# Kernel optimization log

Hardware: AMD Instinct MI355X
Metric: run time of the kernel (lower is better)

The kernel has to match this reference:

```python
import jax, jax.numpy as jnp
import numpy as np

INV_SQRT_4PI = 0.28209479177387814  # 1/sqrt(4*pi)

def sh_l(r, l):
    """Real spherical harmonics of unit vectors r [..., 3], e3nn order,
    'integral' normalization (e3nn o3.spherical_harmonics default)."""
    x, y, z = r[..., 0], r[..., 1], r[..., 2]
    if l == 0:
        return jnp.full(r.shape[:-1] + (1,), INV_SQRT_4PI, r.dtype)
    if l == 1:
        return 0.4886025119029199 * r  # sqrt(3/(4pi)) * (x, y, z)
    s15 = 3.872983346207417 * INV_SQRT_4PI   # sqrt(15)/sqrt(4pi)
    s5 = 2.23606797749979 * INV_SQRT_4PI     # sqrt(5)/sqrt(4pi)
    return jnp.stack([
        s15 * x * z,
        s15 * x * y,
        s5 * (y * y - 0.5 * (x * x + z * z)),
        s15 * y * z,
        0.5 * s15 * (z * z - x * x),
    ], axis=-1)

def layer_norm(x, g, b, eps=1e-5):
    mu = jnp.mean(x, axis=-1, keepdims=True)
    var = jnp.mean((x - mu) ** 2, axis=-1, keepdims=True)
    return (x - mu) * jax.lax.rsqrt(var + eps) * g + b

def setup_inputs() -> dict:
    key = jax.random.key(0)
    N, C, L = 1024, 128, 3  # nodes, sphere_channels, lmax+1
    ks = jax.random.split(key, 12)
    s = 0.02
    return {
        "x_emb": jax.random.normal(ks[0], (N, 9, C), jnp.float32),
        "pos": jax.random.normal(ks[1], (N, 3), jnp.float32) * 3.0,
        "q_w": jax.random.normal(ks[2], (C, C), jnp.float32) * s,
        "q_b": jnp.zeros((C,), jnp.float32),
        "k_w": jax.random.normal(ks[3], (C, C), jnp.float32) * s,
        "k_b": jnp.zeros((C,), jnp.float32),
        "v_w": jax.random.normal(ks[4], (L, C, C), jnp.float32) * s,
        "v_b0": jnp.zeros((C,), jnp.float32),
        "out_w": jax.random.normal(ks[5], (L, C, C), jnp.float32) * s,
        "ln_g": jnp.ones((L, C), jnp.float32),
        "ln_b": jnp.zeros((L, C), jnp.float32),
        "batch": jnp.sort(jax.random.randint(ks[6], (N,), 0, 16)).astype(jnp.int64),
    }

def reference(x_emb, pos, q_w, q_b, k_w, k_b, v_w, v_b0, out_w, ln_g, ln_b, batch):
    N, _, C = x_emb.shape
    H = 8
    D = C // H
    degs = (1, 3, 5)  # 2l+1 for l = 0, 1, 2

    # pairwise unit displacements  [N, N, 3]
    diff = pos[:, None, :] - pos[None, :, :]
    dist = jnp.maximum(jnp.linalg.norm(diff, axis=-1, keepdims=True), 1e-8)
    r_hat = diff / dist

    same = batch[:, None] == batch[None, :]           # [N, N]
    valid = same & ~jnp.eye(N, dtype=bool)

    # per-degree features: split x_emb[:, 9, C] into [1, 3, 5]
    feats = [x_emb[:, 0:1], x_emb[:, 1:4], x_emb[:, 4:9]]

    # HTR invariant pairwise score  [N, N, C]
    score = jnp.zeros((N, N, C), x_emb.dtype)
    for l, f in enumerate(feats):
        sh = sh_l(r_hat, l)                           # [N, N, 2l+1]
        score = score + jnp.einsum('imc,ijm->ijc', f, sh) / degs[l]
    score = score * valid[..., None].astype(score.dtype)

    q = (score.mean(axis=1) @ q_w.T + q_b).reshape(N, H, D)
    k = (score.mean(axis=0) @ k_w.T + k_b).reshape(N, H, D)

    attn = jnp.einsum('ihd,jhd->hij', q, k) * (D ** -0.5)
    attn = jnp.where(same[None], attn, -jnp.inf)
    attn = jnp.nan_to_num(jax.nn.softmax(attn, axis=-1))

    outs = []
    for l, f in enumerate(feats):
        m = degs[l]
        v = f @ v_w[l].T
        if l == 0:
            v = v + v_b0
        v = v.reshape(N, m, H, D)
        o = jnp.einsum('hij,jmhd->imhd', attn, v).reshape(N, m, C)
        o = o @ out_w[l].T
        outs.append(layer_norm(f + o, ln_g[l], ln_b[l]))
    return jnp.concatenate(outs, axis=1)
```

## Files before the change

kernel.cpp:

```cpp
#include <hip/hip_runtime.h>
#include <hip/hip_bf16.h>
#include <math.h>

#define NN 1024

typedef __attribute__((ext_vector_type(8))) short bf16x8;
typedef __attribute__((ext_vector_type(4))) float f32x4;

__device__ __forceinline__ float wave_sum(float v) {
#pragma unroll
  for (int off = 32; off > 0; off >>= 1) v += __shfl_down(v, off);
  return v;
}
__device__ __forceinline__ float wave_max(float v) {
#pragma unroll
  for (int off = 32; off > 0; off >>= 1) v = fmaxf(v, __shfl_down(v, off));
  return v;
}
__device__ __forceinline__ short f2bf(float x) {
  __hip_bfloat16 b = __float2bfloat16(x);
  return *(short*)&b;
}

#define SH_C0 0.28209479177387814f
#define SH_C1 0.4886025119029199f
#define SH_S15 1.0925484305920792f
#define SH_S5 0.6307831305050401f

__global__ __launch_bounds__(256) void htr_geom(
    const float* __restrict__ qw, const float* __restrict__ kw,
    const float* __restrict__ vw, const float* __restrict__ ow,
    const float* __restrict__ x_emb, const float* __restrict__ pos,
    const int* __restrict__ batch, short* __restrict__ wbf,
    short* __restrict__ x_bf, short* __restrict__ fT,
    short* __restrict__ Wsh, short* __restrict__ rowm_bf) {
  const int b = blockIdx.x;
  const int tid = threadIdx.x;
  __shared__ short tile[128][34];
  __shared__ float red[4][9];
  __shared__ float sm[9];

  if (b < 8) {
    const float* src;
    if (b == 0) src = qw;
    else if (b == 1) src = kw;
    else if (b < 5) src = vw + (b - 2) * 16384;
    else src = ow + (b - 5) * 16384;
    short* dst = wbf + b * 16384;
    for (int idx = tid; idx < 16384; idx += 256) dst[idx] = f2bf(src[idx]);
  } else if (b < 1160) {
    int base = (b - 8) * 1024 + tid * 4;
    float4 v = *(const float4*)(x_emb + base);
    *(short4*)(x_bf + base) = make_short4(f2bf(v.x), f2bf(v.y), f2bf(v.z), f2bf(v.w));
  } else if (b < 1448) {
    const int sub = b - 1160;
    const int i0 = (sub & 31) * 32;
    const int m = sub >> 5;
#pragma unroll
    for (int it = 0; it < 16; ++it) {
      int e = tid + it * 256;
      int r = e >> 7, c = e & 127;
      tile[c][r] = f2bf(x_emb[((i0 + r) * 9 + m) * 128 + c]);
    }
    __syncthreads();
#pragma unroll
    for (int it = 0; it < 8; ++it) {
      int idx = tid + it * 256;
      int c = idx >> 4, ii2 = idx & 15;
      *(short2*)(fT + c * 9216 + m * 1024 + i0 + ii2 * 2) =
          make_short2(tile[c][ii2 * 2], tile[c][ii2 * 2 + 1]);
    }
  } else if (b < 2472) {
    const int j = b - 1448;
    const float pjx = pos[j * 3 + 0], pjy = pos[j * 3 + 1], pjz = pos[j * 3 + 2];
    const int bj = batch[j];
    short* wrow = Wsh + j * 9216;
    for (int i = tid; i < 1024; i += 256) {
      float dx = pos[i * 3 + 0] - pjx;
      float dy = pos[i * 3 + 1] - pjy;
      float dz = pos[i * 3 + 2] - pjz;
      bool ok = (i != j) && (batch[i] == bj);
      float okf = ok ? 1.f : 0.f;
      float d2 = dx * dx + dy * dy + dz * dz;
      float inv = okf / fmaxf(sqrtf(d2), 1e-8f);
      float x = dx * inv, y = dy * inv, z = dz * inv;
      wrow[0 * 1024 + i] = f2bf(SH_C0 * okf);
      wrow[1 * 1024 + i] = f2bf((SH_C1 * (1.f / 3.f)) * x);
      wrow[2 * 1024 + i] = f2bf((SH_C1 * (1.f / 3.f)) * y);
      wrow[3 * 1024 + i] = f2bf((SH_C1 * (1.f / 3.f)) * z);
      wrow[4 * 1024 + i] = f2bf((SH_S15 * 0.2f) * x * z);
      wrow[5 * 1024 + i] = f2bf((SH_S15 * 0.2f) * x * y);
      wrow[6 * 1024 + i] = f2bf((SH_S5 * 0.2f) * (y * y - 0.5f * (x * x + z * z)));
      wrow[7 * 1024 + i] = f2bf((SH_S15 * 0.2f) * y * z);
      wrow[8 * 1024 + i] = f2bf((0.5f * SH_S15 * 0.2f) * (z * z - x * x));
    }
  } else {
    const int i = b - 2472;
    const float px = pos[i * 3 + 0], py = pos[i * 3 + 1], pz = pos[i * 3 + 2];
    const int bi = batch[i];
    float s[9];
#pragma unroll
    for (int m = 0; m < 9; ++m) s[m] = 0.f;
    for (int j = tid; j < NN; j += 256) {
      if (j == i) continue;
      if (batch[j] != bi) continue;
      float dx = px - pos[j * 3 + 0];
      float dy = py - pos[j * 3 + 1];
      float dz = pz - pos[j * 3 + 2];
      float d2 = dx * dx + dy * dy + dz * dz;
      float inv = 1.0f / fmaxf(sqrtf(d2), 1e-8f);
      float x = dx * inv, y = dy * inv, z = dz * inv;
      s[0] += 1.0f;
      s[1] += x; s[2] += y; s[3] += z;
      s[4] += x * z; s[5] += x * y;
      s[6] += y * y - 0.5f * (x * x + z * z);
      s[7] += y * z;
      s[8] += z * z - x * x;
    }
    const int wave = tid >> 6, lane = tid & 63;
#pragma unroll
    for (int m = 0; m < 9; ++m) {
      float v = wave_sum(s[m]);
      if (lane == 0) red[wave][m] = v;
    }
    __syncthreads();
    if (tid < 9) {
      float v = red[0][tid] + red[1][tid] + red[2][tid] + red[3][tid];
      float scl = SH_S15 * 0.2f;
      if (tid == 0) scl = SH_C0;
      else if (tid < 4) scl = SH_C1 * (1.f / 3.f);
      else if (tid == 6) scl = SH_S5 * 0.2f;
      else if (tid == 8) scl = 0.5f * SH_S15 * 0.2f;
      sm[tid] = v * scl * (1.0f / 1024.0f);
    }
    __syncthreads();
    if (tid < 128) {
      float acc = 0.f;
#pragma unroll
      for (int m = 0; m < 9; ++m)
        acc = fmaf(sm[m], x_emb[(i * 9 + m) * 128 + tid], acc);
      rowm_bf[i * 128 + tid] = f2bf(acc);
    }
  }
}

#define CMS 16
__global__ __launch_bounds__(64) void htr_colmean_mfma(
    const short* __restrict__ Wsh, const short* __restrict__ fT,
    float* __restrict__ part) {
  const int jbase = blockIdx.x * 16;
  const int ks = blockIdx.y;
  const int lane = threadIdx.x;
  const int q = lane >> 4, l15 = lane & 15;
  const short* ap = Wsh + (jbase + l15) * 9216 + ks * 576 + q * 8;
  const short* bp = fT + l15 * 9216 + ks * 576 + q * 8;
  f32x4 acc[8];
#pragma unroll
  for (int t = 0; t < 8; ++t) acc[t] = (f32x4){0.f, 0.f, 0.f, 0.f};
  bf16x8 a = *(const bf16x8*)ap;
  bf16x8 b[8];
#pragma unroll
  for (int t = 0; t < 8; ++t) b[t] = *(const bf16x8*)(bp + t * 147456);
  for (int s = 1; s < 18; ++s) {
    const int off = s * 32;
    bf16x8 an = *(const bf16x8*)(ap + off);
    bf16x8 bn[8];
#pragma unroll
    for (int t = 0; t < 8; ++t) bn[t] = *(const bf16x8*)(bp + t * 147456 + off);
#pragma unroll
    for (int t = 0; t < 8; ++t)
      acc[t] = __builtin_amdgcn_mfma_f32_16x16x32_bf16(a, b[t], acc[t], 0, 0, 0);
    a = an;
#pragma unroll
    for (int t = 0; t < 8; ++t) b[t] = bn[t];
  }
#pragma unroll
  for (int t = 0; t < 8; ++t)
    acc[t] = __builtin_amdgcn_mfma_f32_16x16x32_bf16(a, b[t], acc[t], 0, 0, 0);
#pragma unroll
  for (int t = 0; t < 8; ++t)
#pragma unroll
    for (int r = 0; r < 4; ++r)
      part[(ks * 1024 + jbase + q * 4 + r) * 128 + t * 16 + l15] = acc[t][r];
}

__global__ __launch_bounds__(64) void htr_proj(
    const short* __restrict__ rowm_bf, const float* __restrict__ part,
    const short* __restrict__ x_bf, const short* __restrict__ wbf,
    const float* __restrict__ q_b, const float* __restrict__ k_b,
    const float* __restrict__ v_b0, float* __restrict__ qbuf,
    float* __restrict__ khbuf, short* __restrict__ vbT) {
  const int ibase = blockIdx.x * 16;
  const int y = blockIdx.y;
  const int lane = threadIdx.x;
  const int q = lane >> 4, l15 = lane & 15;

  bf16x8 a[4];
  const short* bp;
  if (y == 0) {
    const short* ap = rowm_bf + (ibase + l15) * 128 + q * 8;
#pragma unroll
    for (int ks = 0; ks < 4; ++ks) a[ks] = *(const bf16x8*)(ap + ks * 32);
    bp = wbf + l15 * 128 + q * 8;
  } else if (y == 1) {
    const float* pp = part + (size_t)(ibase + l15) * 128;
#pragma unroll
    for (int ks = 0; ks < 4; ++ks) {
      float s0 = 0.f, s1 = 0.f, s2 = 0.f, s3 = 0.f;
      float s4 = 0.f, s5 = 0.f, s6 = 0.f, s7 = 0.f;
#pragma unroll
      for (int s = 0; s < CMS; ++s) {
        const float* ps = pp + s * 131072 + ks * 32 + q * 8;
        float4 u0 = *(const float4*)(ps);
        float4 u1 = *(const float4*)(ps + 4);
        s0 += u0.x; s1 += u0.y; s2 += u0.z; s3 += u0.w;
        s4 += u1.x; s5 += u1.y; s6 += u1.z; s7 += u1.w;
      }
      const float sc = 1.0f / 1024.0f;
      bf16x8 av;
      av[0] = f2bf(s0 * sc); av[1] = f2bf(s1 * sc);
      av[2] = f2bf(s2 * sc); av[3] = f2bf(s3 * sc);
      av[4] = f2bf(s4 * sc); av[5] = f2bf(s5 * sc);
      av[6] = f2bf(s6 * sc); av[7] = f2bf(s7 * sc);
      a[ks] = av;
    }
    bp = wbf + 16384 + l15 * 128 + q * 8;
  } else {
    const int m = y - 2;
    const int l = (m == 0) ? 0 : ((m < 4) ? 1 : 2);
    const short* ap = x_bf + ((ibase + l15) * 9 + m) * 128 + q * 8;
#pragma unroll
    for (int ks = 0; ks < 4; ++ks) a[ks] = *(const bf16x8*)(ap + ks * 32);
    bp = wbf + (2 + l) * 16384 + l15 * 128 + q * 8;
  }

  f32x4 acc[8];
#pragma unroll
  for (int t = 0; t < 8; ++t) {
    acc[t] = (f32x4){0.f, 0.f, 0.f, 0.f};
    const short* bt = bp + t * 2048;
#pragma unroll
    for (int ks = 0; ks < 4; ++ks) {
      bf16x8 b = *(const bf16x8*)(bt + ks * 32);
      acc[t] = __builtin_amdgcn_mfma_f32_16x16x32_bf16(a[ks], b, acc[t], 0, 0, 0);
    }
  }

  if (y == 0) {
#pragma unroll
    for (int t = 0; t < 8; ++t) {
      float bo = q_b[t * 16 + l15];
#pragma unroll
      for (int r = 0; r < 4; ++r)
        qbuf[(ibase + q * 4 + r) * 128 + t * 16 + l15] = acc[t][r] + bo;
    }
  } else if (y == 1) {
#pragma unroll
    for (int t = 0; t < 8; ++t) {
      float bo = k_b[t * 16 + l15];
#pragma unroll
      for (int r = 0; r < 4; ++r)
        khbuf[(t * 1024 + ibase + q * 4 + r) * 16 + l15] = acc[t][r] + bo;
    }
  } else {
    const int m = y - 2;
#pragma unroll
    for (int t = 0; t < 8; ++t) {
      float bias = (m == 0) ? v_b0[t * 16 + l15] : 0.f;
#pragma unroll
      for (int r = 0; r < 4; ++r)
        vbT[(t * 144 + m * 16 + l15) * 1024 + ibase + q * 4 + r] =
            f2bf(acc[t][r] + bias);
    }
  }
}

template <int NT0, int NT>
__device__ __forceinline__ void apply_phase(
    const short* P, const short* __restrict__ vbT,
    short* __restrict__ obuf_bf, int ibase, int h, int lane) {
  const int q = lane >> 4, l15 = lane & 15;
  const int xs = (l15 & 7) << 3;
  const short* pr = P + l15 * 1024;
  const short* bp = vbT + (h * 144 + l15) * 1024 + q * 8;
  f32x4 acc[NT];
#pragma unroll
  for (int t = 0; t < NT; ++t) acc[t] = (f32x4){0.f, 0.f, 0.f, 0.f};
  bf16x8 a = *(const bf16x8*)(pr + ((q * 8) ^ xs));
  bf16x8 b[NT];
#pragma unroll
  for (int t = 0; t < NT; ++t) b[t] = *(const bf16x8*)(bp + (NT0 + t) * 16384);
  for (int ks = 1; ks < 32; ++ks) {
    const int off = ks * 32;
    bf16x8 an = *(const bf16x8*)(pr + ((off + q * 8) ^ xs));
    bf16x8 bn[NT];
#pragma unroll
    for (int t = 0; t < NT; ++t)
      bn[t] = *(const bf16x8*)(bp + (NT0 + t) * 16384 + off);
#pragma unroll
    for (int t = 0; t < NT; ++t)
      acc[t] = __builtin_amdgcn_mfma_f32_16x16x32_bf16(a, b[t], acc[t], 0, 0, 0);
    a = an;
#pragma unroll
    for (int t = 0; t < NT; ++t) b[t] = bn[t];
  }
#pragma unroll
  for (int t = 0; t < NT; ++t)
    acc[t] = __builtin_amdgcn_mfma_f32_16x16x32_bf16(a, b[t], acc[t], 0, 0, 0);
#pragma unroll
  for (int t = 0; t < NT; ++t)
#pragma unroll
    for (int r = 0; r < 4; ++r)
      obuf_bf[((ibase + q * 4 + r) * 9 + NT0 + t) * 128 + h * 16 + l15] =
          f2bf(acc[t][r]);
}

__global__ __launch_bounds__(256) void htr_attn_apply(
    const float* __restrict__ qbuf, const float* __restrict__ khbuf,
    const int* __restrict__ batch, const short* __restrict__ vbT,
    short* __restrict__ obuf_bf) {
  const int ibase = blockIdx.x * 16;
  const int h = blockIdx.y;
  const int tid = threadIdx.x;
  const int w = tid >> 6;
  const int lane = tid & 63;
  __shared__ short P[16 * 1024];

  const int r0 = ibase + w * 4;
  float qr[4][16];
  int bi[4];
#pragma unroll
  for (int r = 0; r < 4; ++r) {
    bi[r] = batch[r0 + r];
    const float* qp = qbuf + (r0 + r) * 128 + h * 16;
#pragma unroll
    for (int d = 0; d < 16; ++d) qr[r][d] = qp[d] * 0.25f;
  }
  float s[4][16];
#pragma unroll
  for (int jt = 0; jt < 16; ++jt) {
    const int j = jt * 64 + lane;
    const int bj = batch[j];
    const float4* kp = (const float4*)(khbuf + (h * 1024 + j) * 16);
    float4 k0 = kp[0], k1 = kp[1], k2 = kp[2], k3 = kp[3];
#pragma unroll
    for (int r = 0; r < 4; ++r) {
      float d = 0.f;
      d = fmaf(qr[r][0], k0.x, d);  d = fmaf(qr[r][1], k0.y, d);
      d = fmaf(qr[r][2], k0.z, d);  d = fmaf(qr[r][3], k0.w, d);
      d = fmaf(qr[r][4], k1.x, d);  d = fmaf(qr[r][5], k1.y, d);
      d = fmaf(qr[r][6], k1.z, d);  d = fmaf(qr[r][7], k1.w, d);
      d = fmaf(qr[r][8], k2.x, d);  d = fmaf(qr[r][9], k2.y, d);
      d = fmaf(qr[r][10], k2.z, d); d = fmaf(qr[r][11], k2.w, d);
      d = fmaf(qr[r][12], k3.x, d); d = fmaf(qr[r][13], k3.y, d);
      d = fmaf(qr[r][14], k3.z, d); d = fmaf(qr[r][15], k3.w, d);
      s[r][jt] = (bj == bi[r]) ? d : -INFINITY;
    }
  }
#pragma unroll
  for (int r = 0; r < 4; ++r) {
    float mx = s[r][0];
#pragma unroll
    for (int jt = 1; jt < 16; ++jt) mx = fmaxf(mx, s[r][jt]);
    mx = wave_max(mx);
    mx = __shfl(mx, 0);
    float t = 0.f;
#pragma unroll
    for (int jt = 0; jt < 16; ++jt) {
      s[r][jt] = expf(s[r][jt] - mx);
      t += s[r][jt];
    }
    t = wave_sum(t);
    t = __shfl(t, 0);
    const float inv = 1.0f / t;
    const int row = w * 4 + r;
    const int xs = (row & 7) << 3;
    short* pw = P + row * 1024;
#pragma unroll
    for (int jt = 0; jt < 16; ++jt) {
      const int j = jt * 64 + lane;
      pw[j ^ xs] = f2bf(s[r][jt] * inv);
    }
  }
  __syncthreads();

  if (w == 0)      apply_phase<0, 3>(P, vbT, obuf_bf, ibase, h, lane);
  else if (w == 1) apply_phase<3, 2>(P, vbT, obuf_bf, ibase, h, lane);
  else if (w == 2) apply_phase<5, 2>(P, vbT, obuf_bf, ibase, h, lane);
  else             apply_phase<7, 2>(P, vbT, obuf_bf, ibase, h, lane);
}

__global__ __launch_bounds__(64) void htr_outln_mfma(
    const short* __restrict__ obuf_bf, const float* __restrict__ x_emb,
    const short* __restrict__ wbf, const float* __restrict__ ln_g,
    const float* __restrict__ ln_b, float* __restrict__ out) {
  const int ibase = blockIdx.x * 16;
  const int m = blockIdx.y;
  const int l = (m == 0) ? 0 : ((m < 4) ? 1 : 2);
  const int lane = threadIdx.x;
  const int q = lane >> 4, l15 = lane & 15;
  const short* ap = obuf_bf + ((ibase + l15) * 9 + m) * 128 + q * 8;
  const short* bp = wbf + (5 + l) * 16384 + l15 * 128 + q * 8;
  bf16x8 a[4];
#pragma unroll
  for (int ks = 0; ks < 4; ++ks) a[ks] = *(const bf16x8*)(ap + ks * 32);
  f32x4 acc[8];
#pragma unroll
  for (int t = 0; t < 8; ++t) {
    acc[t] = (f32x4){0.f, 0.f, 0.f, 0.f};
    const short* bt = bp + t * 2048;
#pragma unroll
    for (int ks = 0; ks < 4; ++ks) {
      bf16x8 b = *(const bf16x8*)(bt + ks * 32);
      acc[t] = __builtin_amdgcn_mfma_f32_16x16x32_bf16(a[ks], b, acc[t], 0, 0, 0);
    }
  }
  float g[8], bb[8];
#pragma unroll
  for (int t = 0; t < 8; ++t) {
    g[t] = ln_g[l * 128 + t * 16 + l15];
    bb[t] = ln_b[l * 128 + t * 16 + l15];
  }
#pragma unroll
  for (int r = 0; r < 4; ++r) {
    const int i = ibase + q * 4 + r;
    const float* xr = x_emb + (i * 9 + m) * 128;
    float v[8];
    float sv = 0.f, sq = 0.f;
#pragma unroll
    for (int t = 0; t < 8; ++t) {
      v[t] = acc[t][r] + xr[t * 16 + l15];
      sv += v[t];
      sq += v[t] * v[t];
    }
#pragma unroll
    for (int off = 1; off < 16; off <<= 1) {
      sv += __shfl_xor(sv, off);
      sq += __shfl_xor(sq, off);
    }
    float mu = sv * (1.f / 128.f);
    float var = sq * (1.f / 128.f) - mu * mu;
    float rs = rsqrtf(var + 1e-5f);
    float* orow = out + (i * 9 + m) * 128;
#pragma unroll
    for (int t = 0; t < 8; ++t)
      orow[t * 16 + l15] = (v[t] - mu) * rs * g[t] + bb[t];
  }
}

extern "C" void kernel_launch(void* const* d_in, const int* in_sizes, int n_in,
                              void* d_out, int out_size, void* d_ws, size_t ws_size,
                              hipStream_t stream) {
  (void)in_sizes; (void)n_in; (void)out_size; (void)ws_size;
  const float* x_emb = (const float*)d_in[0];
  const float* pos   = (const float*)d_in[1];
  const float* q_w   = (const float*)d_in[2];
  const float* q_b   = (const float*)d_in[3];
  const float* k_w   = (const float*)d_in[4];
  const float* k_b   = (const float*)d_in[5];
  const float* v_w   = (const float*)d_in[6];
  const float* v_b0  = (const float*)d_in[7];
  const float* out_w = (const float*)d_in[8];
  const float* ln_g  = (const float*)d_in[9];
  const float* ln_b  = (const float*)d_in[10];
  const int*   batch = (const int*)d_in[11];
  float* out = (float*)d_out;

  float* ws = (float*)d_ws;
  short* rowm_bf = (short*)(ws + 0);
  float* qbuf    = ws + 65536;
  float* khbuf   = ws + 196608;
  short* wbf     = (short*)(ws + 327680);
  short* x_bf    = (short*)(ws + 393216);
  short* vbT     = (short*)(ws + 983040);
  short* obuf_bf = (short*)(ws + 1572864);
  float* part    = ws + 2162688;
  short* Wsh     = (short*)(ws + 6356992);
  short* fT      = (short*)(ws + 11075584);

  htr_geom<<<3496, 256, 0, stream>>>(q_w, k_w, v_w, out_w, x_emb, pos, batch,
                                     wbf, x_bf, fT, Wsh, rowm_bf);
  htr_colmean_mfma<<<dim3(64, CMS), 64, 0, stream>>>(Wsh, fT, part);
  htr_proj<<<dim3(64, 11), 64, 0, stream>>>(rowm_bf, part, x_bf, wbf, q_b, k_b,
                                            v_b0, qbuf, khbuf, vbT);
  htr_attn_apply<<<dim3(64, 8), 256, 0, stream>>>(qbuf, khbuf, batch, vbT,
                                                  obuf_bf);
  htr_outln_mfma<<<dim3(64, 9), 64, 0, stream>>>(obuf_bf, x_emb, wbf, ln_g,
                                                 ln_b, out);
}
```

Before: 157.7 us.

## Compute spherical-harmonic weights on the fly inside column-mean MFMA kernel

Measured after the change: 192.2 us. 21.8% more time.

```diff
diff --git a/kernel.cpp b/kernel.cpp
--- a/kernel.cpp
+++ b/kernel.cpp
@@ -33,7 +33,7 @@
     const float* __restrict__ x_emb, const float* __restrict__ pos,
     const int* __restrict__ batch, short* __restrict__ wbf,
     short* __restrict__ x_bf, short* __restrict__ fT,
-    short* __restrict__ Wsh, short* __restrict__ rowm_bf) {
+    short* __restrict__ rowm_bf) {
   const int b = blockIdx.x;
   const int tid = threadIdx.x;
   __shared__ short tile[128][34];
@@ -70,32 +70,8 @@
       *(short2*)(fT + c * 9216 + m * 1024 + i0 + ii2 * 2) =
           make_short2(tile[c][ii2 * 2], tile[c][ii2 * 2 + 1]);
     }
-  } else if (b < 2472) {
-    const int j = b - 1448;
-    const float pjx = pos[j * 3 + 0], pjy = pos[j * 3 + 1], pjz = pos[j * 3 + 2];
-    const int bj = batch[j];
-    short* wrow = Wsh + j * 9216;
-    for (int i = tid; i < 1024; i += 256) {
-      float dx = pos[i * 3 + 0] - pjx;
-      float dy = pos[i * 3 + 1] - pjy;
-      float dz = pos[i * 3 + 2] - pjz;
-      bool ok = (i != j) && (batch[i] == bj);
-      float okf = ok ? 1.f : 0.f;
-      float d2 = dx * dx + dy * dy + dz * dz;
-      float inv = okf / fmaxf(sqrtf(d2), 1e-8f);
-      float x = dx * inv, y = dy * inv, z = dz * inv;
-      wrow[0 * 1024 + i] = f2bf(SH_C0 * okf);
-      wrow[1 * 1024 + i] = f2bf((SH_C1 * (1.f / 3.f)) * x);
-      wrow[2 * 1024 + i] = f2bf((SH_C1 * (1.f / 3.f)) * y);
-      wrow[3 * 1024 + i] = f2bf((SH_C1 * (1.f / 3.f)) * z);
-      wrow[4 * 1024 + i] = f2bf((SH_S15 * 0.2f) * x * z);
-      wrow[5 * 1024 + i] = f2bf((SH_S15 * 0.2f) * x * y);
-      wrow[6 * 1024 + i] = f2bf((SH_S5 * 0.2f) * (y * y - 0.5f * (x * x + z * z)));
-      wrow[7 * 1024 + i] = f2bf((SH_S15 * 0.2f) * y * z);
-      wrow[8 * 1024 + i] = f2bf((0.5f * SH_S15 * 0.2f) * (z * z - x * x));
-    }
   } else {
-    const int i = b - 2472;
+    const int i = b - 1448;
     const float px = pos[i * 3 + 0], py = pos[i * 3 + 1], pz = pos[i * 3 + 2];
     const int bi = batch[i];
     float s[9];
@@ -146,37 +122,86 @@
 
 #define CMS 16
 __global__ __launch_bounds__(64) void htr_colmean_mfma(
-    const short* __restrict__ Wsh, const short* __restrict__ fT,
-    float* __restrict__ part) {
+    const float* __restrict__ pos, const int* __restrict__ batch,
+    const short* __restrict__ fT, float* __restrict__ part) {
   const int jbase = blockIdx.x * 16;
   const int ks = blockIdx.y;
   const int lane = threadIdx.x;
   const int q = lane >> 4, l15 = lane & 15;
-  const short* ap = Wsh + (jbase + l15) * 9216 + ks * 576 + q * 8;
+  __shared__ float4 pb[1024];
+  for (int i = lane; i < 1024; i += 64)
+    pb[i] = make_float4(pos[i * 3 + 0], pos[i * 3 + 1], pos[i * 3 + 2],
+                        __int_as_float(batch[i]));
+  __syncthreads();
+
+  const int j = jbase + l15;
+  const float4 pj = pb[j];
+  const int bj = __float_as_int(pj.w);
   const short* bp = fT + l15 * 9216 + ks * 576 + q * 8;
+
   f32x4 acc[8];
 #pragma unroll
   for (int t = 0; t < 8; ++t) acc[t] = (f32x4){0.f, 0.f, 0.f, 0.f};
-  bf16x8 a = *(const bf16x8*)ap;
   bf16x8 b[8];
 #pragma unroll
   for (int t = 0; t < 8; ++t) b[t] = *(const bf16x8*)(bp + t * 147456);
-  for (int s = 1; s < 18; ++s) {
-    const int off = s * 32;
-    bf16x8 an = *(const bf16x8*)(ap + off);
+
+  for (int s = 0; s < 18; ++s) {
     bf16x8 bn[8];
-#pragma unroll
-    for (int t = 0; t < 8; ++t) bn[t] = *(const bf16x8*)(bp + t * 147456 + off);
+    if (s < 17) {
+      const int off = (s + 1) * 32;
+#pragma unroll
+      for (int t = 0; t < 8; ++t) bn[t] = *(const bf16x8*)(bp + t * 147456 + off);
+    }
+    const int k0 = ks * 576 + s * 32;
+    const int m = k0 >> 10;
+    const int ib = (k0 & 1023) + q * 8;
+    bf16x8 av;
+    if (m == 0) {
+#pragma unroll
+      for (int t = 0; t < 8; ++t) {
+        const int e = (t + q) & 7;
+        const int i = ib + e;
+        const float4 pi = pb[i];
+        const bool ok = (i != j) && (__float_as_int(pi.w) == bj);
+        av[e] = f2bf(SH_C0 * (ok ? 1.f : 0.f));
+      }
+    } else {
+#pragma unroll
+      for (int t = 0; t < 8; ++t) {
+        const int e = (t + q) & 7;
+        const int i = ib + e;
+        const float4 pi = pb[i];
+        const bool ok = (i != j) && (__float_as_int(pi.w) == bj);
+        const float okf = ok ? 1.f : 0.f;
+        const float dx = pi.x - pj.x;
+        const float dy = pi.y - pj.y;
+        const float dz = pi.z - pj.z;
+        const float d2 = dx * dx + dy * dy + dz * dz;
+        const float inv = okf / fmaxf(sqrtf(d2), 1e-8f);
+        const float x = dx * inv, y = dy * inv, z = dz * inv;
+        float v;
+        switch (m) {
+          case 1: v = (SH_C1 * (1.f / 3.f)) * x; break;
+          case 2: v = (SH_C1 * (1.f / 3.f)) * y; break;
+          case 3: v = (SH_C1 * (1.f / 3.f)) * z; break;
+          case 4: v = (SH_S15 * 0.2f) * x * z; break;
+          case 5: v = (SH_S15 * 0.2f) * x * y; break;
+          case 6: v = (SH_S5 * 0.2f) * (y * y - 0.5f * (x * x + z * z)); break;
+          case 7: v = (SH_S15 * 0.2f) * y * z; break;
+          default: v = (0.5f * SH_S15 * 0.2f) * (z * z - x * x); break;
+        }
+        av[e] = f2bf(v);
+      }
+    }
 #pragma unroll
     for (int t = 0; t < 8; ++t)
-      acc[t] = __builtin_amdgcn_mfma_f32_16x16x32_bf16(a, b[t], acc[t], 0, 0, 0);
-    a = an;
-#pragma unroll
-    for (int t = 0; t < 8; ++t) b[t] = bn[t];
-  }
-#pragma unroll
-  for (int t = 0; t < 8; ++t)
-    acc[t] = __builtin_amdgcn_mfma_f32_16x16x32_bf16(a, b[t], acc[t], 0, 0, 0);
+      acc[t] = __builtin_amdgcn_mfma_f32_16x16x32_bf16(av, b[t], acc[t], 0, 0, 0);
+    if (s < 17) {
+#pragma unroll
+      for (int t = 0; t < 8; ++t) b[t] = bn[t];
+    }
+  }
 #pragma unroll
   for (int t = 0; t < 8; ++t)
 #pragma unroll
@@ -475,12 +500,11 @@
   short* vbT     = (short*)(ws + 983040);
   short* obuf_bf = (short*)(ws + 1572864);
   float* part    = ws + 2162688;
-  short* Wsh     = (short*)(ws + 6356992);
   short* fT      = (short*)(ws + 11075584);
 
-  htr_geom<<<3496, 256, 0, stream>>>(q_w, k_w, v_w, out_w, x_emb, pos, batch,
-                                     wbf, x_bf, fT, Wsh, rowm_bf);
-  htr_colmean_mfma<<<dim3(64, CMS), 64, 0, stream>>>(Wsh, fT, part);
+  htr_geom<<<2472, 256, 0, stream>>>(q_w, k_w, v_w, out_w, x_emb, pos, batch,
+                                     wbf, x_bf, fT, rowm_bf);
+  htr_colmean_mfma<<<dim3(64, CMS), 64, 0, stream>>>(pos, batch, fT, part);
   htr_proj<<<dim3(64, 11), 64, 0, stream>>>(rowm_bf, part, x_bf, wbf, q_b, k_b,
                                             v_b0, qbuf, khbuf, vbT);
   htr_attn_apply<<<dim3(64, 8), 256, 0, stream>>>(qbuf, khbuf, batch, vbT,
```

## Stage shared B tile in LDS across four waves in colmean MFMA kernel

Applied to the files above, without the earlier changes.

After: 152.7 us. 3.2% less time.

```diff
diff --git a/kernel.cpp b/kernel.cpp
--- a/kernel.cpp
+++ b/kernel.cpp
@@ -145,43 +145,54 @@
 }
 
 #define CMS 16
-__global__ __launch_bounds__(64) void htr_colmean_mfma(
+__global__ __launch_bounds__(256) void htr_colmean_mfma(
     const short* __restrict__ Wsh, const short* __restrict__ fT,
     float* __restrict__ part) {
-  const int jbase = blockIdx.x * 16;
+  const int jb = blockIdx.x * 64;
   const int ks = blockIdx.y;
-  const int lane = threadIdx.x;
+  const int tid = threadIdx.x;
+  const int w = tid >> 6, lane = tid & 63;
   const int q = lane >> 4, l15 = lane & 15;
-  const short* ap = Wsh + (jbase + l15) * 9216 + ks * 576 + q * 8;
-  const short* bp = fT + l15 * 9216 + ks * 576 + q * 8;
+  __shared__ short bt[32][584];
+
+  const int j = jb + w * 16 + l15;
+  const short* ap = Wsh + j * 9216 + ks * 576 + q * 8;
+  bf16x8 A[18];
+#pragma unroll
+  for (int s = 0; s < 18; ++s) A[s] = *(const bf16x8*)(ap + s * 32);
+
   f32x4 acc[8];
 #pragma unroll
   for (int t = 0; t < 8; ++t) acc[t] = (f32x4){0.f, 0.f, 0.f, 0.f};
-  bf16x8 a = *(const bf16x8*)ap;
-  bf16x8 b[8];
-#pragma unroll
-  for (int t = 0; t < 8; ++t) b[t] = *(const bf16x8*)(bp + t * 147456);
-  for (int s = 1; s < 18; ++s) {
-    const int off = s * 32;
-    bf16x8 an = *(const bf16x8*)(ap + off);
-    bf16x8 bn[8];
-#pragma unroll
-    for (int t = 0; t < 8; ++t) bn[t] = *(const bf16x8*)(bp + t * 147456 + off);
-#pragma unroll
-    for (int t = 0; t < 8; ++t)
-      acc[t] = __builtin_amdgcn_mfma_f32_16x16x32_bf16(a, b[t], acc[t], 0, 0, 0);
-    a = an;
-#pragma unroll
-    for (int t = 0; t < 8; ++t) b[t] = bn[t];
+
+  for (int tc = 0; tc < 4; ++tc) {
+    __syncthreads();
+#pragma unroll
+    for (int it = 0; it < 9; ++it) {
+      int idx = tid + it * 256;
+      int c = idx / 72;
+      int g = idx - c * 72;
+      *(bf16x8*)(&bt[c][g * 8]) =
+          *(const bf16x8*)(fT + (tc * 32 + c) * 9216 + ks * 576 + g * 8);
+    }
+    __syncthreads();
+#pragma unroll
+    for (int tl = 0; tl < 2; ++tl) {
+      const int t = tc * 2 + tl;
+      const short* brow = &bt[tl * 16 + l15][q * 8];
+#pragma unroll
+      for (int s = 0; s < 18; ++s) {
+        bf16x8 b = *(const bf16x8*)(brow + s * 32);
+        acc[t] = __builtin_amdgcn_mfma_f32_16x16x32_bf16(A[s], b, acc[t], 0, 0, 0);
+      }
+    }
   }
 #pragma unroll
   for (int t = 0; t < 8; ++t)
-    acc[t] = __builtin_amdgcn_mfma_f32_16x16x32_bf16(a, b[t], acc[t], 0, 0, 0);
-#pragma unroll
-  for (int t = 0; t < 8; ++t)
 #pragma unroll
     for (int r = 0; r < 4; ++r)
-      part[(ks * 1024 + jbase + q * 4 + r) * 128 + t * 16 + l15] = acc[t][r];
+      part[(ks * 1024 + jb + w * 16 + q * 4 + r) * 128 + t * 16 + l15] =
+          acc[t][r];
 }
 
 __global__ __launch_bounds__(64) void htr_proj(
@@ -480,7 +491,7 @@
 
   htr_geom<<<3496, 256, 0, stream>>>(q_w, k_w, v_w, out_w, x_emb, pos, batch,
                                      wbf, x_bf, fT, Wsh, rowm_bf);
-  htr_colmean_mfma<<<dim3(64, CMS), 64, 0, stream>>>(Wsh, fT, part);
+  htr_colmean_mfma<<<dim3(16, CMS), 256, 0, stream>>>(Wsh, fT, part);
   htr_proj<<<dim3(64, 11), 64, 0, stream>>>(rowm_bf, part, x_bf, wbf, q_b, k_b,
                                             v_b0, qbuf, khbuf, vbT);
   htr_attn_apply<<<dim3(64, 8), 256, 0, stream>>>(qbuf, khbuf, batch, vbT,
```
